# Kernel optimization log

Measured on AMD Instinct MI355X. Metric: run time of the kernel, lower is better.

## Reference

```python
import jax, jax.numpy as jnp
import numpy as np

B, N, T, E = 8, 10000, 12, 160000
C_IN, C_SP, C_OUT, K = 32, 64, 64, 3
EPS = 1e-5

def _conv1xk(x, w, b, pad):
    # x: (B, Cin, N, T), w: (Cout, Cin, 1, k) -- conv only along time axis
    y = jax.lax.conv_general_dilated(x, w, (1, 1), [(0, 0), (pad, pad)],
                                     dimension_numbers=('NCHW', 'OIHW', 'NCHW'))
    return y + b[None, :, None, None]

def _temporal_block(x, w, b, gamma, beta, mean, var):
    out = _conv1xk(x, w, b, pad=1)
    p, q = jnp.split(out, 2, axis=1)
    out = p * jax.nn.sigmoid(q)  # GLU gate
    scale = gamma * jax.lax.rsqrt(var + EPS)  # eval-mode BatchNorm2d
    return (out - mean[None, :, None, None]) * scale[None, :, None, None] + beta[None, :, None, None]

def _cheb_conv(x, edge_index, edge_weight, W, b):
    # x: (BT, N, C). PyG ChebConv, sym normalization, lambda_max=2 =>
    # Lhat = -D^{-1/2} A D^{-1/2} (zero diagonal). Recursion T0=x, T1=Lhat x,
    # Tk = 2 Lhat T_{k-1} - T_{k-2}; out = sum_k Tk @ W_k + b.
    row, col = edge_index[0], edge_index[1]
    n = x.shape[1]
    deg = jnp.zeros((n,), x.dtype).at[row].add(edge_weight)
    deg_safe = jnp.where(deg > 0, deg, 1.0)
    dinv = jnp.where(deg > 0, jax.lax.rsqrt(deg_safe), 0.0)
    norm = -edge_weight * dinv[row] * dinv[col]  # (E,)

    def lhat(z):
        msg = z[:, row, :] * norm[None, :, None]          # gather + scale
        return jnp.zeros_like(z).at[:, col, :].add(msg)   # scatter-add

    Tx0 = x
    out = jnp.einsum('bnc,cd->bnd', Tx0, W[0])
    Tx1 = lhat(x)
    out = out + jnp.einsum('bnc,cd->bnd', Tx1, W[1])
    for k in range(2, W.shape[0]):
        Tx2 = 2.0 * lhat(Tx1) - Tx0
        out = out + jnp.einsum('bnc,cd->bnd', Tx2, W[k])
        Tx0, Tx1 = Tx1, Tx2
    return out + b

def setup_inputs():
    key = jax.random.key(0)
    ks = jax.random.split(key, 16)
    s = 0.05
    return {
        'x': jax.random.normal(ks[0], (B, C_IN, N, T), jnp.float32),
        'edge_index': jax.random.randint(ks[1], (2, E), 0, N),
        'edge_weight': jax.random.uniform(ks[2], (E,), jnp.float32),
        'w_gate1': jax.random.normal(ks[3], (2 * C_SP, C_IN, 1, 3), jnp.float32) * s,
        'b_gate1': jnp.zeros((2 * C_SP,), jnp.float32),
        'bn1_gamma': 1.0 + 0.1 * jax.random.normal(ks[4], (C_SP,), jnp.float32),
        'bn1_beta': 0.1 * jax.random.normal(ks[5], (C_SP,), jnp.float32),
        'bn1_mean': 0.1 * jax.random.normal(ks[6], (C_SP,), jnp.float32),
        'bn1_var': jax.random.uniform(ks[7], (C_SP,), jnp.float32, 0.5, 1.5),
        'cheb_w': jax.random.normal(ks[8], (K, C_SP, C_SP), jnp.float32) * s,
        'cheb_b': jnp.zeros((C_SP,), jnp.float32),
        'ln_gamma': jnp.ones((C_SP,), jnp.float32),
        'ln_beta': jnp.zeros((C_SP,), jnp.float32),
        'w_gate2': jax.random.normal(ks[9], (2 * C_OUT, C_SP, 1, 3), jnp.float32) * s,
        'b_gate2': jnp.zeros((2 * C_OUT,), jnp.float32),
        'bn2_gamma': 1.0 + 0.1 * jax.random.normal(ks[10], (C_OUT,), jnp.float32),
        'bn2_beta': 0.1 * jax.random.normal(ks[11], (C_OUT,), jnp.float32),
        'bn2_mean': 0.1 * jax.random.normal(ks[12], (C_OUT,), jnp.float32),
        'bn2_var': jax.random.uniform(ks[13], (C_OUT,), jnp.float32, 0.5, 1.5),
        'w_res': jax.random.normal(ks[14], (C_OUT, C_IN, 1, 1), jnp.float32) * s,
        'b_res': jnp.zeros((C_OUT,), jnp.float32),
    }

def reference(x, edge_index, edge_weight, w_gate1, b_gate1, bn1_gamma, bn1_beta, bn1_mean, bn1_var,
              cheb_w, cheb_b, ln_gamma, ln_beta, w_gate2, b_gate2, bn2_gamma, bn2_beta, bn2_mean,
              bn2_var, w_res, b_res):
    b_, _, n_, t_ = x.shape
    res = _conv1xk(x, w_res, b_res, pad=0)  # 1x1 residual projection
    out = _temporal_block(x, w_gate1, b_gate1, bn1_gamma, bn1_beta, bn1_mean, bn1_var)
    c_s = out.shape[1]
    # (B, C_s, N, T) -> (B*T, N, C_s): spatial graph conv per time snapshot
    h = out.transpose(0, 3, 2, 1).reshape(b_ * t_, n_, c_s)
    h = _cheb_conv(h, edge_index, edge_weight, cheb_w, cheb_b)
    mu = h.mean(-1, keepdims=True)
    var = ((h - mu) ** 2).mean(-1, keepdims=True)
    h = (h - mu) * jax.lax.rsqrt(var + EPS) * ln_gamma + ln_beta  # LayerNorm
    h = jax.nn.relu(h)
    h = h.reshape(b_, t_, n_, c_s).transpose(0, 3, 2, 1)
    out = _temporal_block(h, w_gate2, b_gate2, bn2_gamma, bn2_beta, bn2_mean, bn2_var)
    return out + res
```

## Files before the change

kernel.cpp:

```cpp
#include <hip/hip_runtime.h>
#include <math.h>

#define BB 8
#define CIN 32
#define NN 10000
#define TTT 12
#define EE 160000
#define CSP 64
#define BT (BB*TTT)
#define NPAIR 48
#define EPSV 1e-5f

typedef __attribute__((ext_vector_type(8))) short bf16x8;
typedef __attribute__((ext_vector_type(4))) float f32x4;

static __device__ __forceinline__ float sigmoidf_(float v) {
    return __builtin_amdgcn_rcpf(1.f + __expf(-v));
}

static __device__ __forceinline__ short f2bf(float v) {
    unsigned u = __float_as_uint(v);
    u = (u + 0x7fffu + ((u >> 16) & 1u)) >> 16;
    return (short)u;
}
static __device__ __forceinline__ float lo16f(unsigned u) {
    return __uint_as_float(u << 16);
}
static __device__ __forceinline__ float hi16f(unsigned u) {
    return __uint_as_float(u & 0xffff0000u);
}
static __device__ __forceinline__ unsigned packbf(float a, float b) {
    return ((unsigned)(ushort)f2bf(a)) | (((unsigned)(ushort)f2bf(b)) << 16);
}

__global__ void k_deg(const int* __restrict__ ei, const float* __restrict__ ew,
                      float* __restrict__ deg) {
    int e = blockIdx.x * 256 + threadIdx.x;
    if (e < EE) atomicAdd(&deg[ei[e]], ew[e]);
}

__global__ void k_dinv(float* __restrict__ deg) {
    int n = blockIdx.x * 256 + threadIdx.x;
    if (n < NN) { float d = deg[n]; deg[n] = d > 0.f ? rsqrtf(d) : 0.f; }
}

__global__ void k_norm_cnt(const int* __restrict__ ei, const float* __restrict__ ew,
                           const float* __restrict__ dinv, float* __restrict__ nrm,
                           int* __restrict__ cnt) {
    int e = blockIdx.x * 256 + threadIdx.x;
    if (e < EE) {
        int r = ei[e], c = ei[EE + e];
        nrm[e] = -ew[e] * dinv[r] * dinv[c];
        atomicAdd(&cnt[c], 1);
    }
}

__global__ void k_scan(const int* __restrict__ cnt, int* __restrict__ offs,
                       int* __restrict__ cursor) {
    __shared__ int sh[1024];
    int tid = threadIdx.x;
    int running = 0;
    for (int base = 0; base < NN; base += 1024) {
        int i = base + tid;
        int v = (i < NN) ? cnt[i] : 0;
        sh[tid] = v;
        __syncthreads();
        for (int off = 1; off < 1024; off <<= 1) {
            int t = (tid >= off) ? sh[tid - off] : 0;
            __syncthreads();
            sh[tid] += t;
            __syncthreads();
        }
        int incl = sh[tid];
        if (i < NN) { offs[i] = running + incl - v; cursor[i] = running + incl - v; }
        int ct = sh[1023];
        __syncthreads();
        running += ct;
    }
    if (tid == 0) offs[NN] = running;
}

__global__ void k_fill(const int* __restrict__ ei, const float* __restrict__ nrm,
                       int* __restrict__ cursor, unsigned* __restrict__ csrp) {
    int e = blockIdx.x * 256 + threadIdx.x;
    if (e < EE) {
        int cdst = ei[EE + e];
        int p = atomicAdd(&cursor[cdst], 1);
        csrp[p] = (((unsigned)(ushort)f2bf(nrm[e])) << 16) | (unsigned)ei[e];
    }
}

__global__ void k_cvt_w(const float* __restrict__ wg1, const float* __restrict__ wg2,
                        const float* __restrict__ wr, const float* __restrict__ cwf,
                        short* __restrict__ wtap1, short* __restrict__ wtap2,
                        short* __restrict__ o3, short* __restrict__ wt02,
                        short* __restrict__ wt1, short* __restrict__ wt2) {
    int i = blockIdx.x * 256 + threadIdx.x;
    if (i < 12288) {
        int kk = i / 4096, r = i % 4096, cc = r >> 5, ci = r & 31;
        wtap1[i] = f2bf(wg1[cc * 96 + ci * 3 + kk]);
    }
    if (i < 24576) {
        int kk = i / 8192, r = i % 8192, cc = r >> 6, c = r & 63;
        wtap2[i] = f2bf(wg2[cc * 192 + c * 3 + kk]);
    }
    if (i < 2048)  o3[i] = f2bf(wr[i]);
    if (i < 4096) {
        int cout = i >> 6, cin = i & 63;
        float w0 = cwf[cin * 64 + cout];
        float w1 = cwf[4096 + cin * 64 + cout];
        float w2 = cwf[8192 + cin * 64 + cout];
        wt02[i] = f2bf(w0 - w2);
        wt1[i]  = f2bf(w1);
        wt2[i]  = f2bf(w2);
    }
}

__global__ __launch_bounds__(256, 6) void k_tconv1_mfma(
    const float* __restrict__ x, const short* __restrict__ wtap,
    const float* __restrict__ bg, const float* __restrict__ gam,
    const float* __restrict__ bet, const float* __restrict__ mean,
    const float* __restrict__ var, ushort* __restrict__ h1)
{
    __shared__ short Hs[4][14][40];
    int bi = blockIdx.x;
    int b = bi / 2500;
    int n0 = (bi % 2500) * 4;
    int tid = threadIdx.x;

    if (tid < 128) {
        int n = tid >> 5, ci = tid & 31;
        const float* xp = x + ((size_t)(b * CIN + ci) * NN + n0 + n) * 12;
        float4 a0 = *(const float4*)(xp);
        float4 a1 = *(const float4*)(xp + 4);
        float4 a2 = *(const float4*)(xp + 8);
        short* d = &Hs[n][0][ci];
        d[0] = 0; d[13 * 40] = 0;
        d[1 * 40] = f2bf(a0.x); d[2 * 40] = f2bf(a0.y); d[3 * 40] = f2bf(a0.z);
        d[4 * 40] = f2bf(a0.w); d[5 * 40] = f2bf(a1.x); d[6 * 40] = f2bf(a1.y);
        d[7 * 40] = f2bf(a1.z); d[8 * 40] = f2bf(a1.w); d[9 * 40] = f2bf(a2.x);
        d[10 * 40] = f2bf(a2.y); d[11 * 40] = f2bf(a2.z); d[12 * 40] = f2bf(a2.w);
    }
    __syncthreads();

    int w = tid >> 6, l = tid & 63, lr = l & 15, lq = l >> 4;
    int nct[3], tct[3];
#pragma unroll
    for (int ct = 0; ct < 3; ++ct) {
        int col = ct * 16 + lr;
        nct[ct] = col / 12; tct[ct] = col % 12;
    }
    f32x4 aP[3], aQ[3];
#pragma unroll
    for (int m = 0; m < 3; ++m) { aP[m] = (f32x4){0,0,0,0}; aQ[m] = (f32x4){0,0,0,0}; }

#pragma unroll
    for (int kk = 0; kk < 3; ++kk) {
        bf16x8 wp = *(const bf16x8*)(wtap + ((kk * 128 + w * 16 + lr) * 32 + lq * 8));
        bf16x8 wq = *(const bf16x8*)(wtap + ((kk * 128 + 64 + w * 16 + lr) * 32 + lq * 8));
#pragma unroll
        for (int ct = 0; ct < 3; ++ct) {
            bf16x8 im = *(const bf16x8*)&Hs[nct[ct]][tct[ct] + kk][lq * 8];
            aP[ct] = __builtin_amdgcn_mfma_f32_16x16x32_bf16(im, wp, aP[ct], 0, 0, 0);
            aQ[ct] = __builtin_amdgcn_mfma_f32_16x16x32_bf16(im, wq, aQ[ct], 0, 0, 0);
        }
    }

    int c = w * 16 + lr;
    float bp = bg[c], bq = bg[64 + c];
    float sc = gam[c] * rsqrtf(var[c] + EPSV);
    float mn = mean[c], be = bet[c];
#pragma unroll
    for (int mt = 0; mt < 3; ++mt) {
#pragma unroll
        for (int j = 0; j < 4; ++j) {
            int row = mt * 16 + lq * 4 + j;
            int n = n0 + row / 12, t = row % 12;
            float h = (aP[mt][j] + bp) * sigmoidf_(aQ[mt][j] + bq);
            h1[((size_t)(b * 6 + (t >> 1)) * NN + n) * 128 + (t & 1) * 64 + c] =
                (ushort)f2bf((h - mn) * sc + be);
        }
    }
}

__global__ __launch_bounds__(256, 8) void k_spatial(
    const ushort* __restrict__ h1, const int* __restrict__ offs,
    const unsigned* __restrict__ csr,
    const short* __restrict__ wt02, const short* __restrict__ wt1,
    const short* __restrict__ wt2, const float* __restrict__ cb,
    ushort* __restrict__ O, ushort* __restrict__ U)
{
    __shared__ short Al[64][72];
    __shared__ short Gl[64][72];
    int tid = threadIdx.x;
    int bi = blockIdx.x;
    int xcd = bi & 7, r = bi >> 3;
    int jp = r / 313, ck = r - jp * 313;
    int pair = xcd * 6 + jp;
    int n0 = ck * 32;

    const char* hp = (const char*)h1 + (size_t)pair * NN * 256;
    int w = tid >> 6, l = tid & 63;
    int snap = l >> 5, cp = l & 31;
    unsigned loff = (unsigned)(snap * 128 + cp * 4);

#pragma unroll
    for (int p = 0; p < 8; ++p) {
        int nl = p * 4 + w;
        int n = n0 + nl;
        float a0 = 0.f, a1 = 0.f, b0 = 0.f, b1 = 0.f;
        unsigned sv = 0;
        if (n < NN) {
            sv = *(const unsigned*)(hp + (((unsigned)n) << 8) + loff);
            int o0 = __builtin_amdgcn_readfirstlane(offs[n]);
            int o1 = __builtin_amdgcn_readfirstlane(offs[n + 1]);
            int i = o0;
            for (; i + 7 < o1; i += 8) {
                unsigned e0 = csr[i], e1 = csr[i+1], e2 = csr[i+2], e3 = csr[i+3];
                unsigned e4 = csr[i+4], e5 = csr[i+5], e6 = csr[i+6], e7 = csr[i+7];
                unsigned r0 = *(const unsigned*)(hp + ((e0 & 0xffffu) << 8) + loff);
                unsigned r1 = *(const unsigned*)(hp + ((e1 & 0xffffu) << 8) + loff);
                unsigned r2 = *(const unsigned*)(hp + ((e2 & 0xffffu) << 8) + loff);
                unsigned r3 = *(const unsigned*)(hp + ((e3 & 0xffffu) << 8) + loff);
                unsigned r4 = *(const unsigned*)(hp + ((e4 & 0xffffu) << 8) + loff);
                unsigned r5 = *(const unsigned*)(hp + ((e5 & 0xffffu) << 8) + loff);
                unsigned r6 = *(const unsigned*)(hp + ((e6 & 0xffffu) << 8) + loff);
                unsigned r7 = *(const unsigned*)(hp + ((e7 & 0xffffu) << 8) + loff);
                float w0 = hi16f(e0), w1 = hi16f(e1), w2 = hi16f(e2), w3 = hi16f(e3);
                float w4 = hi16f(e4), w5 = hi16f(e5), w6 = hi16f(e6), w7 = hi16f(e7);
                a0 = fmaf(w0, lo16f(r0), a0); a1 = fmaf(w0, hi16f(r0), a1);
                b0 = fmaf(w1, lo16f(r1), b0); b1 = fmaf(w1, hi16f(r1), b1);
                a0 = fmaf(w2, lo16f(r2), a0); a1 = fmaf(w2, hi16f(r2), a1);
                b0 = fmaf(w3, lo16f(r3), b0); b1 = fmaf(w3, hi16f(r3), b1);
                a0 = fmaf(w4, lo16f(r4), a0); a1 = fmaf(w4, hi16f(r4), a1);
                b0 = fmaf(w5, lo16f(r5), b0); b1 = fmaf(w5, hi16f(r5), b1);
                a0 = fmaf(w6, lo16f(r6), a0); a1 = fmaf(w6, hi16f(r6), a1);
                b0 = fmaf(w7, lo16f(r7), b0); b1 = fmaf(w7, hi16f(r7), b1);
            }
            for (; i + 3 < o1; i += 4) {
                unsigned e0 = csr[i], e1 = csr[i+1], e2 = csr[i+2], e3 = csr[i+3];
                unsigned r0 = *(const unsigned*)(hp + ((e0 & 0xffffu) << 8) + loff);
                unsigned r1 = *(const unsigned*)(hp + ((e1 & 0xffffu) << 8) + loff);
                unsigned r2 = *(const unsigned*)(hp + ((e2 & 0xffffu) << 8) + loff);
                unsigned r3 = *(const unsigned*)(hp + ((e3 & 0xffffu) << 8) + loff);
                float w0 = hi16f(e0), w1 = hi16f(e1), w2 = hi16f(e2), w3 = hi16f(e3);
                a0 = fmaf(w0, lo16f(r0), a0); a1 = fmaf(w0, hi16f(r0), a1);
                b0 = fmaf(w1, lo16f(r1), b0); b1 = fmaf(w1, hi16f(r1), b1);
                a0 = fmaf(w2, lo16f(r2), a0); a1 = fmaf(w2, hi16f(r2), a1);
                b0 = fmaf(w3, lo16f(r3), b0); b1 = fmaf(w3, hi16f(r3), b1);
            }
            for (; i < o1; ++i) {
                unsigned e = csr[i];
                unsigned rr = *(const unsigned*)(hp + ((e & 0xffffu) << 8) + loff);
                float ww = hi16f(e);
                a0 = fmaf(ww, lo16f(rr), a0); a1 = fmaf(ww, hi16f(rr), a1);
            }
        }
        int row = snap * 32 + nl;
        *(unsigned*)&Al[row][cp * 2] = sv;
        *(unsigned*)&Gl[row][cp * 2] = packbf(a0 + b0, a1 + b1);
    }
    __syncthreads();

    int lr = l & 15, lq = l >> 4;
    bf16x8 af[2], gf[2];
#pragma unroll
    for (int ks = 0; ks < 2; ++ks) {
        af[ks] = *(const bf16x8*)&Al[w * 16 + lr][ks * 32 + lq * 8];
        gf[ks] = *(const bf16x8*)&Gl[w * 16 + lr][ks * 32 + lq * 8];
    }
    f32x4 ao[4], au[4];
#pragma unroll
    for (int ct = 0; ct < 4; ++ct) { ao[ct] = (f32x4){0,0,0,0}; au[ct] = (f32x4){0,0,0,0}; }
#pragma unroll
    for (int ct = 0; ct < 4; ++ct) {
#pragma unroll
        for (int ks = 0; ks < 2; ++ks) {
            int woff = (ct * 16 + lr) * 64 + ks * 32 + lq * 8;
            bf16x8 b02 = *(const bf16x8*)(wt02 + woff);
            bf16x8 b1  = *(const bf16x8*)(wt1 + woff);
            bf16x8 b2  = *(const bf16x8*)(wt2 + woff);
            ao[ct] = __builtin_amdgcn_mfma_f32_16x16x32_bf16(af[ks], b02, ao[ct], 0, 0, 0);
            ao[ct] = __builtin_amdgcn_mfma_f32_16x16x32_bf16(gf[ks], b1,  ao[ct], 0, 0, 0);
            au[ct] = __builtin_amdgcn_mfma_f32_16x16x32_bf16(gf[ks], b2,  au[ct], 0, 0, 0);
        }
    }
    __syncthreads();

#pragma unroll
    for (int ct = 0; ct < 4; ++ct) {
        float bb = cb[ct * 16 + lr];
#pragma unroll
        for (int j2 = 0; j2 < 4; ++j2) {
            int rowo = w * 16 + lq * 4 + j2;
            Al[rowo][ct * 16 + lr] = f2bf(ao[ct][j2] + bb);
            Gl[rowo][ct * 16 + lr] = f2bf(au[ct][j2]);
        }
    }
    __syncthreads();

    size_t obase = (size_t)pair * NN * 128;
#pragma unroll
    for (int rr2 = 0; rr2 < 2; ++rr2) {
        int idx = tid + rr2 * 256;
        int node = idx >> 4, part = idx & 15;
        int sn = part >> 3, seg = part & 7;
        int n = n0 + node;
        if (n < NN) {
            size_t off = obase + (size_t)n * 128 + sn * 64 + seg * 8;
            __builtin_nontemporal_store(*(const bf16x8*)&Al[sn * 32 + node][seg * 8],
                                        (bf16x8*)(O + off));
            __builtin_nontemporal_store(*(const bf16x8*)&Gl[sn * 32 + node][seg * 8],
                                        (bf16x8*)(U + off));
        }
    }
}

__global__ __launch_bounds__(256, 8) void k_gather2_ln(
    const ushort* __restrict__ O, const ushort* __restrict__ U,
    const int* __restrict__ offs, const unsigned* __restrict__ csr,
    const float* __restrict__ lng, const float* __restrict__ lnb,
    ushort* __restrict__ hln)
{
    int bi = blockIdx.x;
    int xcd = bi & 7, r = bi >> 3;
    int jp = r / 625, ck = r - jp * 625;
    int pair = xcd * 6 + jp;
    int ng = ck * 16;
    int tid = threadIdx.x;
    int w = tid >> 6, l = tid & 63;
    int snap = l >> 5, cp = l & 31;
    unsigned loff = (unsigned)(snap * 128 + cp * 4);
    const char* up = (const char*)U + (size_t)pair * NN * 256;
    const char* op = (const char*)O + (size_t)pair * NN * 256;
    ushort* hlp = hln + (size_t)pair * NN * 128;

    float2 gv = ((const float2*)lng)[cp];
    float2 bv = ((const float2*)lnb)[cp];

#pragma unroll
    for (int p = 0; p < 4; ++p) {
        int n = ng + p * 4 + w;
        float a0 = 0.f, a1 = 0.f, b0 = 0.f, b1 = 0.f;
        int o0 = __builtin_amdgcn_readfirstlane(offs[n]);
        int o1 = __builtin_amdgcn_readfirstlane(offs[n + 1]);
        int i = o0;
        for (; i + 7 < o1; i += 8) {
            unsigned e0 = csr[i], e1 = csr[i+1], e2 = csr[i+2], e3 = csr[i+3];
            unsigned e4 = csr[i+4], e5 = csr[i+5], e6 = csr[i+6], e7 = csr[i+7];
            unsigned r0 = *(const unsigned*)(up + ((e0 & 0xffffu) << 8) + loff);
            unsigned r1 = *(const unsigned*)(up + ((e1 & 0xffffu) << 8) + loff);
            unsigned r2 = *(const unsigned*)(up + ((e2 & 0xffffu) << 8) + loff);
            unsigned r3 = *(const unsigned*)(up + ((e3 & 0xffffu) << 8) + loff);
            unsigned r4 = *(const unsigned*)(up + ((e4 & 0xffffu) << 8) + loff);
            unsigned r5 = *(const unsigned*)(up + ((e5 & 0xffffu) << 8) + loff);
            unsigned r6 = *(const unsigned*)(up + ((e6 & 0xffffu) << 8) + loff);
            unsigned r7 = *(const unsigned*)(up + ((e7 & 0xffffu) << 8) + loff);
            float w0 = hi16f(e0), w1 = hi16f(e1), w2 = hi16f(e2), w3 = hi16f(e3);
            float w4 = hi16f(e4), w5 = hi16f(e5), w6 = hi16f(e6), w7 = hi16f(e7);
            a0 = fmaf(w0, lo16f(r0), a0); a1 = fmaf(w0, hi16f(r0), a1);
            b0 = fmaf(w1, lo16f(r1), b0); b1 = fmaf(w1, hi16f(r1), b1);
            a0 = fmaf(w2, lo16f(r2), a0); a1 = fmaf(w2, hi16f(r2), a1);
            b0 = fmaf(w3, lo16f(r3), b0); b1 = fmaf(w3, hi16f(r3), b1);
            a0 = fmaf(w4, lo16f(r4), a0); a1 = fmaf(w4, hi16f(r4), a1);
            b0 = fmaf(w5, lo16f(r5), b0); b1 = fmaf(w5, hi16f(r5), b1);
            a0 = fmaf(w6, lo16f(r6), a0); a1 = fmaf(w6, hi16f(r6), a1);
            b0 = fmaf(w7, lo16f(r7), b0); b1 = fmaf(w7, hi16f(r7), b1);
        }
        for (; i + 3 < o1; i += 4) {
            unsigned e0 = csr[i], e1 = csr[i+1], e2 = csr[i+2], e3 = csr[i+3];
            unsigned r0 = *(const unsigned*)(up + ((e0 & 0xffffu) << 8) + loff);
            unsigned r1 = *(const unsigned*)(up + ((e1 & 0xffffu) << 8) + loff);
            unsigned r2 = *(const unsigned*)(up + ((e2 & 0xffffu) << 8) + loff);
            unsigned r3 = *(const unsigned*)(up + ((e3 & 0xffffu) << 8) + loff);
            float w0 = hi16f(e0), w1 = hi16f(e1), w2 = hi16f(e2), w3 = hi16f(e3);
            a0 = fmaf(w0, lo16f(r0), a0); a1 = fmaf(w0, hi16f(r0), a1);
            b0 = fmaf(w1, lo16f(r1), b0); b1 = fmaf(w1, hi16f(r1), b1);
            a0 = fmaf(w2, lo16f(r2), a0); a1 = fmaf(w2, hi16f(r2), a1);
            b0 = fmaf(w3, lo16f(r3), b0); b1 = fmaf(w3, hi16f(r3), b1);
        }
        for (; i < o1; ++i) {
            unsigned e = csr[i];
            unsigned rr = *(const unsigned*)(up + ((e & 0xffffu) << 8) + loff);
            float ww = hi16f(e);
            a0 = fmaf(ww, lo16f(rr), a0); a1 = fmaf(ww, hi16f(rr), a1);
        }
        unsigned ov = *(const unsigned*)(op + (((unsigned)n) << 8) + loff);
        float acc0 = lo16f(ov) + 2.f * (a0 + b0);
        float acc1 = hi16f(ov) + 2.f * (a1 + b1);
        float s1 = acc0 + acc1;
        float s2 = acc0 * acc0 + acc1 * acc1;
#pragma unroll
        for (int m = 16; m >= 1; m >>= 1) {
            s1 += __shfl_xor(s1, m);
            s2 += __shfl_xor(s2, m);
        }
        float mu = s1 * (1.f / 64.f);
        float vr = s2 * (1.f / 64.f) - mu * mu;
        float rstd = rsqrtf(vr + EPSV);
        float y0 = fmaxf((acc0 - mu) * rstd * gv.x + bv.x, 0.f);
        float y1 = fmaxf((acc1 - mu) * rstd * gv.y + bv.y, 0.f);
        __builtin_nontemporal_store(packbf(y0, y1),
            (unsigned*)(hlp + (size_t)n * 128 + snap * 64 + cp * 2));
    }
}

__global__ __launch_bounds__(256, 4) void k_tconv2_mfma(
    const ushort* __restrict__ hln, const float* __restrict__ x,
    const short* __restrict__ wtap, const short* __restrict__ wrbf,
    const float* __restrict__ bg, const float* __restrict__ gam,
    const float* __restrict__ bet, const float* __restrict__ mean,
    const float* __restrict__ var, const float* __restrict__ bres,
    float* __restrict__ out)
{
    __shared__ short Hs[4][14][72];
    __shared__ short Bx[48 * 40];
    int bi = blockIdx.x;
    int b = bi / 2500;
    int n0 = (bi % 2500) * 4;
    int tid = threadIdx.x;

    for (int j = tid; j < 384; j += 256) {
        int n = j / 96, rem = j % 96;
        int p = rem >> 4, seg = rem & 15;
        bf16x8 v = *(const bf16x8*)(hln + ((size_t)(b * 6 + p) * NN + n0 + n) * 128 + seg * 8);
        *(bf16x8*)&Hs[n][1 + 2 * p + (seg >> 3)][(seg & 7) * 8] = v;
    }
    if (tid < 64) {
        int n = tid >> 4, pt = tid & 15;
        bf16x8 z = (bf16x8){0,0,0,0,0,0,0,0};
        *(bf16x8*)&Hs[n][(pt >> 3) * 13][(pt & 7) * 8] = z;
    }
    for (int j = tid; j < 384; j += 256) {
        int ci = j / 12, r = j - ci * 12;
        const float* xp = x + ((size_t)(b * CIN + ci) * NN + n0) * 12 + r * 4;
        float4 v = *(const float4*)xp;
        float vv[4] = {v.x, v.y, v.z, v.w};
#pragma unroll
        for (int e = 0; e < 4; ++e) {
            int col = r * 4 + e;
            Bx[col * 40 + ci] = f2bf(vv[e]);
        }
    }
    __syncthreads();

    int w = tid >> 6, l = tid & 63, lr = l & 15, lq = l >> 4;
    int nct[3], tct[3];
#pragma unroll
    for (int ct = 0; ct < 3; ++ct) {
        int col = ct * 16 + lr;
        nct[ct] = col / 12; tct[ct] = col % 12;
    }
    f32x4 accP[3], accQ[3], accR[3];
#pragma unroll
    for (int m = 0; m < 3; ++m) {
        accP[m] = (f32x4){0,0,0,0}; accQ[m] = (f32x4){0,0,0,0}; accR[m] = (f32x4){0,0,0,0};
    }

#pragma unroll
    for (int kk = 0; kk < 3; ++kk) {
#pragma unroll
        for (int ks = 0; ks < 2; ++ks) {
            bf16x8 aP = *(const bf16x8*)(wtap + ((kk * 128 + w * 16 + lr) * 64 + ks * 32 + lq * 8));
            bf16x8 aQ = *(const bf16x8*)(wtap + ((kk * 128 + 64 + w * 16 + lr) * 64 + ks * 32 + lq * 8));
#pragma unroll
            for (int ct = 0; ct < 3; ++ct) {
                bf16x8 bfr = *(const bf16x8*)&Hs[nct[ct]][tct[ct] + kk][ks * 32 + lq * 8];
                accP[ct] = __builtin_amdgcn_mfma_f32_16x16x32_bf16(aP, bfr, accP[ct], 0, 0, 0);
                accQ[ct] = __builtin_amdgcn_mfma_f32_16x16x32_bf16(aQ, bfr, accQ[ct], 0, 0, 0);
            }
        }
    }
    {
        bf16x8 aR = *(const bf16x8*)(wrbf + ((w * 16 + lr) * 32 + lq * 8));
#pragma unroll
        for (int ct = 0; ct < 3; ++ct) {
            bf16x8 bx = *(const bf16x8*)(&Bx[(ct * 16 + lr) * 40 + lq * 8]);
            accR[ct] = __builtin_amdgcn_mfma_f32_16x16x32_bf16(aR, bx, accR[ct], 0, 0, 0);
        }
    }

    float bpv[4], bqv[4], scv[4], mnv[4], bev[4], brv[4];
#pragma unroll
    for (int j = 0; j < 4; ++j) {
        int cj = w * 16 + lq * 4 + j;
        bpv[j] = bg[cj]; bqv[j] = bg[64 + cj];
        scv[j] = gam[cj] * rsqrtf(var[cj] + EPSV);
        mnv[j] = mean[cj]; bev[j] = bet[cj]; brv[j] = bres[cj];
    }
#pragma unroll
    for (int ct = 0; ct < 3; ++ct) {
        int col = ct * 16 + lr;
        int n = n0 + col / 12, t = col % 12;
#pragma unroll
        for (int j = 0; j < 4; ++j) {
            int cj = w * 16 + lq * 4 + j;
            float h = (accP[ct][j] + bpv[j]) * sigmoidf_(accQ[ct][j] + bqv[j]);
            float o = (h - mnv[j]) * scv[j] + bev[j] + accR[ct][j] + brv[j];
            __builtin_nontemporal_store(o, &out[((size_t)(b * 64 + cj) * NN + n) * 12 + t]);
        }
    }
}

extern "C" void kernel_launch(void* const* d_in, const int* in_sizes, int n_in,
                              void* d_out, int out_size, void* d_ws, size_t ws_size,
                              hipStream_t stream)
{
    const float* x   = (const float*)d_in[0];
    const int*   ei  = (const int*)d_in[1];
    const float* ew  = (const float*)d_in[2];
    const float* wg1 = (const float*)d_in[3];
    const float* bg1 = (const float*)d_in[4];
    const float* g1  = (const float*)d_in[5];
    const float* be1 = (const float*)d_in[6];
    const float* m1  = (const float*)d_in[7];
    const float* v1  = (const float*)d_in[8];
    const float* cw  = (const float*)d_in[9];
    const float* cb  = (const float*)d_in[10];
    const float* lng = (const float*)d_in[11];
    const float* lnb = (const float*)d_in[12];
    const float* wg2 = (const float*)d_in[13];
    const float* bg2 = (const float*)d_in[14];
    const float* g2  = (const float*)d_in[15];
    const float* be2 = (const float*)d_in[16];
    const float* m2  = (const float*)d_in[17];
    const float* v2  = (const float*)d_in[18];
    const float* wr  = (const float*)d_in[19];
    const float* br  = (const float*)d_in[20];

    char* w = (char*)d_ws;
    short* wtap1 = (short*)w;  w += 12288 * 2;
    short* wtap2 = (short*)w;  w += 24576 * 2;
    short* wrbf  = (short*)w;  w += 2048 * 2;
    short* wt02  = (short*)w;  w += 4096 * 2;
    short* wt1   = (short*)w;  w += 4096 * 2;
    short* wt2   = (short*)w;  w += 4096 * 2;
    ushort* h1   = (ushort*)w; w += (size_t)NPAIR * NN * 128 * 2;
    ushort* O    = (ushort*)w; w += (size_t)NPAIR * NN * 128 * 2;
    float* deg   = (float*)w;  w += NN * 4;
    int*   cnt   = (int*)w;    w += NN * 4;
    int*   offs  = (int*)w;    w += (NN + 1) * 4;
    int*   cursor= (int*)w;    w += NN * 4;
    float* nrm   = (float*)w;  w += EE * 4;
    unsigned* csr = (unsigned*)w; w += EE * 4;
    ushort* U = (ushort*)d_out;

    hipMemsetAsync(deg, 0, NN * 4 * 2, stream);

    k_deg<<<625, 256, 0, stream>>>(ei, ew, deg);
    k_dinv<<<40, 256, 0, stream>>>(deg);
    k_norm_cnt<<<625, 256, 0, stream>>>(ei, ew, deg, nrm, cnt);
    k_scan<<<1, 1024, 0, stream>>>(cnt, offs, cursor);
    k_fill<<<625, 256, 0, stream>>>(ei, nrm, cursor, csr);
    k_cvt_w<<<96, 256, 0, stream>>>(wg1, wg2, wr, cw, wtap1, wtap2, wrbf, wt02, wt1, wt2);

    k_tconv1_mfma<<<BB * 2500, 256, 0, stream>>>(x, wtap1, bg1, g1, be1, m1, v1, h1);
    k_spatial<<<8 * 6 * 313, 256, 0, stream>>>(h1, offs, csr, wt02, wt1, wt2, cb, O, U);
    k_gather2_ln<<<8 * 6 * 625, 256, 0, stream>>>(O, U, offs, csr, lng, lnb, h1);
    k_tconv2_mfma<<<BB * 2500, 256, 0, stream>>>(h1, x, wtap2, wrbf, bg2, g2, be2, m2, v2, br,
                                                 (float*)d_out);
}
```

Measured before the change: 818.5 us.

## Split edge neighbors across wave halves with 8-byte row gathers

Result: slower. 906.7 us (+10.8%).

```diff
diff --git a/kernel.cpp b/kernel.cpp
--- a/kernel.cpp
+++ b/kernel.cpp
@@ -183,6 +183,24 @@
     }
 }
 
+#define PAIR2(PTR, PV, A0, A1, A2, A3)                                        \
+    {                                                                          \
+        unsigned e = half ? (PV).y : (PV).x;                                   \
+        uint2 rv = *(const uint2*)((PTR) + ((e & 0xffffu) << 8) + loff2);      \
+        float ww = hi16f(e);                                                   \
+        A0 = fmaf(ww, lo16f(rv.x), A0); A1 = fmaf(ww, hi16f(rv.x), A1);        \
+        A2 = fmaf(ww, lo16f(rv.y), A2); A3 = fmaf(ww, hi16f(rv.y), A3);        \
+    }
+
+#define SINGLE1(PTR, I, A0, A1, A2, A3)                                       \
+    {                                                                          \
+        unsigned e = csr[I];                                                   \
+        uint2 rv = *(const uint2*)((PTR) + ((e & 0xffffu) << 8) + loff2);      \
+        float ww = half ? 0.f : hi16f(e);                                      \
+        A0 = fmaf(ww, lo16f(rv.x), A0); A1 = fmaf(ww, hi16f(rv.x), A1);        \
+        A2 = fmaf(ww, lo16f(rv.y), A2); A3 = fmaf(ww, hi16f(rv.y), A3);        \
+    }
+
 __global__ __launch_bounds__(256, 8) void k_spatial(
     const ushort* __restrict__ h1, const int* __restrict__ offs,
     const unsigned* __restrict__ csr,
@@ -201,64 +219,49 @@
 
     const char* hp = (const char*)h1 + (size_t)pair * NN * 256;
     int w = tid >> 6, l = tid & 63;
-    int snap = l >> 5, cp = l & 31;
-    unsigned loff = (unsigned)(snap * 128 + cp * 4);
+    int half = l >> 5, sub = l & 31;
+    unsigned loff2 = (unsigned)(sub * 8);
 
 #pragma unroll
     for (int p = 0; p < 8; ++p) {
         int nl = p * 4 + w;
         int n = n0 + nl;
-        float a0 = 0.f, a1 = 0.f, b0 = 0.f, b1 = 0.f;
-        unsigned sv = 0;
+        float a0 = 0.f, a1 = 0.f, a2 = 0.f, a3 = 0.f;
+        float b0 = 0.f, b1 = 0.f, b2 = 0.f, b3 = 0.f;
+        uint2 sv = {0u, 0u};
         if (n < NN) {
-            sv = *(const unsigned*)(hp + (((unsigned)n) << 8) + loff);
-            int o0 = __builtin_amdgcn_readfirstlane(offs[n]);
+            sv = *(const uint2*)(hp + (((unsigned)n) << 8) + loff2);
+            int i  = __builtin_amdgcn_readfirstlane(offs[n]);
             int o1 = __builtin_amdgcn_readfirstlane(offs[n + 1]);
-            int i = o0;
+            if ((i & 1) && i < o1) { SINGLE1(hp, i, a0, a1, a2, a3); ++i; }
             for (; i + 7 < o1; i += 8) {
-                unsigned e0 = csr[i], e1 = csr[i+1], e2 = csr[i+2], e3 = csr[i+3];
-                unsigned e4 = csr[i+4], e5 = csr[i+5], e6 = csr[i+6], e7 = csr[i+7];
-                unsigned r0 = *(const unsigned*)(hp + ((e0 & 0xffffu) << 8) + loff);
-                unsigned r1 = *(const unsigned*)(hp + ((e1 & 0xffffu) << 8) + loff);
-                unsigned r2 = *(const unsigned*)(hp + ((e2 & 0xffffu) << 8) + loff);
-                unsigned r3 = *(const unsigned*)(hp + ((e3 & 0xffffu) << 8) + loff);
-                unsigned r4 = *(const unsigned*)(hp + ((e4 & 0xffffu) << 8) + loff);
-                unsigned r5 = *(const unsigned*)(hp + ((e5 & 0xffffu) << 8) + loff);
-                unsigned r6 = *(const unsigned*)(hp + ((e6 & 0xffffu) << 8) + loff);
-                unsigned r7 = *(const unsigned*)(hp + ((e7 & 0xffffu) << 8) + loff);
-                float w0 = hi16f(e0), w1 = hi16f(e1), w2 = hi16f(e2), w3 = hi16f(e3);
-                float w4 = hi16f(e4), w5 = hi16f(e5), w6 = hi16f(e6), w7 = hi16f(e7);
-                a0 = fmaf(w0, lo16f(r0), a0); a1 = fmaf(w0, hi16f(r0), a1);
-                b0 = fmaf(w1, lo16f(r1), b0); b1 = fmaf(w1, hi16f(r1), b1);
-                a0 = fmaf(w2, lo16f(r2), a0); a1 = fmaf(w2, hi16f(r2), a1);
-                b0 = fmaf(w3, lo16f(r3), b0); b1 = fmaf(w3, hi16f(r3), b1);
-                a0 = fmaf(w4, lo16f(r4), a0); a1 = fmaf(w4, hi16f(r4), a1);
-                b0 = fmaf(w5, lo16f(r5), b0); b1 = fmaf(w5, hi16f(r5), b1);
-                a0 = fmaf(w6, lo16f(r6), a0); a1 = fmaf(w6, hi16f(r6), a1);
-                b0 = fmaf(w7, lo16f(r7), b0); b1 = fmaf(w7, hi16f(r7), b1);
+                uint2 p0 = *(const uint2*)(csr + i);
+                uint2 p1 = *(const uint2*)(csr + i + 2);
+                uint2 p2 = *(const uint2*)(csr + i + 4);
+                uint2 p3 = *(const uint2*)(csr + i + 6);
+                PAIR2(hp, p0, a0, a1, a2, a3);
+                PAIR2(hp, p1, b0, b1, b2, b3);
+                PAIR2(hp, p2, a0, a1, a2, a3);
+                PAIR2(hp, p3, b0, b1, b2, b3);
             }
-            for (; i + 3 < o1; i += 4) {
-                unsigned e0 = csr[i], e1 = csr[i+1], e2 = csr[i+2], e3 = csr[i+3];
-                unsigned r0 = *(const unsigned*)(hp + ((e0 & 0xffffu) << 8) + loff);
-                unsigned r1 = *(const unsigned*)(hp + ((e1 & 0xffffu) << 8) + loff);
-                unsigned r2 = *(const unsigned*)(hp + ((e2 & 0xffffu) << 8) + loff);
-                unsigned r3 = *(const unsigned*)(hp + ((e3 & 0xffffu) << 8) + loff);
-                float w0 = hi16f(e0), w1 = hi16f(e1), w2 = hi16f(e2), w3 = hi16f(e3);
-                a0 = fmaf(w0, lo16f(r0), a0); a1 = fmaf(w0, hi16f(r0), a1);
-                b0 = fmaf(w1, lo16f(r1), b0); b1 = fmaf(w1, hi16f(r1), b1);
-                a0 = fmaf(w2, lo16f(r2), a0); a1 = fmaf(w2, hi16f(r2), a1);
-                b0 = fmaf(w3, lo16f(r3), b0); b1 = fmaf(w3, hi16f(r3), b1);
+            for (; i + 1 < o1; i += 2) {
+                uint2 p0 = *(const uint2*)(csr + i);
+                PAIR2(hp, p0, a0, a1, a2, a3);
             }
-            for (; i < o1; ++i) {
-                unsigned e = csr[i];
-                unsigned rr = *(const unsigned*)(hp + ((e & 0xffffu) << 8) + loff);
-                float ww = hi16f(e);
-                a0 = fmaf(ww, lo16f(rr), a0); a1 = fmaf(ww, hi16f(rr), a1);
-            }
-        }
-        int row = snap * 32 + nl;
-        *(unsigned*)&Al[row][cp * 2] = sv;
-        *(unsigned*)&Gl[row][cp * 2] = packbf(a0 + b0, a1 + b1);
+            if (i < o1) SINGLE1(hp, i, a0, a1, a2, a3);
+        }
+        float t0 = a0 + b0, t1 = a1 + b1, t2 = a2 + b2, t3 = a3 + b3;
+        t0 += __shfl_xor(t0, 32);
+        t1 += __shfl_xor(t1, 32);
+        t2 += __shfl_xor(t2, 32);
+        t3 += __shfl_xor(t3, 32);
+        if (half == 0) {
+            int rowo = (sub >> 4) * 32 + nl;
+            int chg = sub & 15;
+            *(uint2*)&Al[rowo][chg * 4] = sv;
+            uint2 gp = { packbf(t0, t1), packbf(t2, t3) };
+            *(uint2*)&Gl[rowo][chg * 4] = gp;
+        }
     }
     __syncthreads();
 
@@ -329,79 +332,72 @@
     int ng = ck * 16;
     int tid = threadIdx.x;
     int w = tid >> 6, l = tid & 63;
-    int snap = l >> 5, cp = l & 31;
-    unsigned loff = (unsigned)(snap * 128 + cp * 4);
+    int half = l >> 5, sub = l & 31;
+    unsigned loff2 = (unsigned)(sub * 8);
     const char* up = (const char*)U + (size_t)pair * NN * 256;
     const char* op = (const char*)O + (size_t)pair * NN * 256;
     ushort* hlp = hln + (size_t)pair * NN * 128;
 
-    float2 gv = ((const float2*)lng)[cp];
-    float2 bv = ((const float2*)lnb)[cp];
+    int c0i = sub * 2;
+    float2 gva = ((const float2*)lng)[c0i & 31];
+    float2 gvb = ((const float2*)lng)[(c0i + 1) & 31];
+    float2 bva = ((const float2*)lnb)[c0i & 31];
+    float2 bvb = ((const float2*)lnb)[(c0i + 1) & 31];
 
 #pragma unroll
     for (int p = 0; p < 4; ++p) {
         int n = ng + p * 4 + w;
-        float a0 = 0.f, a1 = 0.f, b0 = 0.f, b1 = 0.f;
-        int o0 = __builtin_amdgcn_readfirstlane(offs[n]);
+        float a0 = 0.f, a1 = 0.f, a2 = 0.f, a3 = 0.f;
+        float b0 = 0.f, b1 = 0.f, b2 = 0.f, b3 = 0.f;
+        int i  = __builtin_amdgcn_readfirstlane(offs[n]);
         int o1 = __builtin_amdgcn_readfirstlane(offs[n + 1]);
-        int i = o0;
+        if ((i & 1) && i < o1) { SINGLE1(up, i, a0, a1, a2, a3); ++i; }
         for (; i + 7 < o1; i += 8) {
-            unsigned e0 = csr[i], e1 = csr[i+1], e2 = csr[i+2], e3 = csr[i+3];
-            unsigned e4 = csr[i+4], e5 = csr[i+5], e6 = csr[i+6], e7 = csr[i+7];
-            unsigned r0 = *(const unsigned*)(up + ((e0 & 0xffffu) << 8) + loff);
-            unsigned r1 = *(const unsigned*)(up + ((e1 & 0xffffu) << 8) + loff);
-            unsigned r2 = *(const unsigned*)(up + ((e2 & 0xffffu) << 8) + loff);
-            unsigned r3 = *(const unsigned*)(up + ((e3 & 0xffffu) << 8) + loff);
-            unsigned r4 = *(const unsigned*)(up + ((e4 & 0xffffu) << 8) + loff);
-            unsigned r5 = *(const unsigned*)(up + ((e5 & 0xffffu) << 8) + loff);
-            unsigned r6 = *(const unsigned*)(up + ((e6 & 0xffffu) << 8) + loff);
-            unsigned r7 = *(const unsigned*)(up + ((e7 & 0xffffu) << 8) + loff);
-            float w0 = hi16f(e0), w1 = hi16f(e1), w2 = hi16f(e2), w3 = hi16f(e3);
-            float w4 = hi16f(e4), w5 = hi16f(e5), w6 = hi16f(e6), w7 = hi16f(e7);
-            a0 = fmaf(w0, lo16f(r0), a0); a1 = fmaf(w0, hi16f(r0), a1);
-            b0 = fmaf(w1, lo16f(r1), b0); b1 = fmaf(w1, hi16f(r1), b1);
-            a0 = fmaf(w2, lo16f(r2), a0); a1 = fmaf(w2, hi16f(r2), a1);
-            b0 = fmaf(w3, lo16f(r3), b0); b1 = fmaf(w3, hi16f(r3), b1);
-            a0 = fmaf(w4, lo16f(r4), a0); a1 = fmaf(w4, hi16f(r4), a1);
-            b0 = fmaf(w5, lo16f(r5), b0); b1 = fmaf(w5, hi16f(r5), b1);
-            a0 = fmaf(w6, lo16f(r6), a0); a1 = fmaf(w6, hi16f(r6), a1);
-            b0 = fmaf(w7, lo16f(r7), b0); b1 = fmaf(w7, hi16f(r7), b1);
-        }
-        for (; i + 3 < o1; i += 4) {
-            unsigned e0 = csr[i], e1 = csr[i+1], e2 = csr[i+2], e3 = csr[i+3];
-            unsigned r0 = *(const unsigned*)(up + ((e0 & 0xffffu) << 8) + loff);
-            unsigned r1 = *(const unsigned*)(up + ((e1 & 0xffffu) << 8) + loff);
-            unsigned r2 = *(const unsigned*)(up + ((e2 & 0xffffu) << 8) + loff);
-            unsigned r3 = *(const unsigned*)(up + ((e3 & 0xffffu) << 8) + loff);
-            float w0 = hi16f(e0), w1 = hi16f(e1), w2 = hi16f(e2), w3 = hi16f(e3);
-            a0 = fmaf(w0, lo16f(r0), a0); a1 = fmaf(w0, hi16f(r0), a1);
-            b0 = fmaf(w1, lo16f(r1), b0); b1 = fmaf(w1, hi16f(r1), b1);
-            a0 = fmaf(w2, lo16f(r2), a0); a1 = fmaf(w2, hi16f(r2), a1);
-            b0 = fmaf(w3, lo16f(r3), b0); b1 = fmaf(w3, hi16f(r3), b1);
-        }
-        for (; i < o1; ++i) {
-            unsigned e = csr[i];
-            unsigned rr = *(const unsigned*)(up + ((e & 0xffffu) << 8) + loff);
-            float ww = hi16f(e);
-            a0 = fmaf(ww, lo16f(rr), a0); a1 = fmaf(ww, hi16f(rr), a1);
-        }
-        unsigned ov = *(const unsigned*)(op + (((unsigned)n) << 8) + loff);
-        float acc0 = lo16f(ov) + 2.f * (a0 + b0);
-        float acc1 = hi16f(ov) + 2.f * (a1 + b1);
-        float s1 = acc0 + acc1;
-        float s2 = acc0 * acc0 + acc1 * acc1;
-#pragma unroll
-        for (int m = 16; m >= 1; m >>= 1) {
+            uint2 p0 = *(const uint2*)(csr + i);
+            uint2 p1 = *(const uint2*)(csr + i + 2);
+            uint2 p2 = *(const uint2*)(csr + i + 4);
+            uint2 p3 = *(const uint2*)(csr + i + 6);
+            PAIR2(up, p0, a0, a1, a2, a3);
+            PAIR2(up, p1, b0, b1, b2, b3);
+            PAIR2(up, p2, a0, a1, a2, a3);
+            PAIR2(up, p3, b0, b1, b2, b3);
+        }
+        for (; i + 1 < o1; i += 2) {
+            uint2 p0 = *(const uint2*)(csr + i);
+            PAIR2(up, p0, a0, a1, a2, a3);
+        }
+        if (i < o1) SINGLE1(up, i, a0, a1, a2, a3);
+
+        float g0 = a0 + b0, g1 = a1 + b1, g2 = a2 + b2, g3 = a3 + b3;
+        g0 += __shfl_xor(g0, 32);
+        g1 += __shfl_xor(g1, 32);
+        g2 += __shfl_xor(g2, 32);
+        g3 += __shfl_xor(g3, 32);
+
+        uint2 ov = *(const uint2*)(op + (((unsigned)n) << 8) + loff2);
+        float acc0 = lo16f(ov.x) + 2.f * g0;
+        float acc1 = hi16f(ov.x) + 2.f * g1;
+        float acc2 = lo16f(ov.y) + 2.f * g2;
+        float acc3 = hi16f(ov.y) + 2.f * g3;
+        float s1 = (acc0 + acc1) + (acc2 + acc3);
+        float s2 = (acc0 * acc0 + acc1 * acc1) + (acc2 * acc2 + acc3 * acc3);
+#pragma unroll
+        for (int m = 8; m >= 1; m >>= 1) {
             s1 += __shfl_xor(s1, m);
             s2 += __shfl_xor(s2, m);
         }
         float mu = s1 * (1.f / 64.f);
         float vr = s2 * (1.f / 64.f) - mu * mu;
         float rstd = rsqrtf(vr + EPSV);
-        float y0 = fmaxf((acc0 - mu) * rstd * gv.x + bv.x, 0.f);
-        float y1 = fmaxf((acc1 - mu) * rstd * gv.y + bv.y, 0.f);
-        __builtin_nontemporal_store(packbf(y0, y1),
-            (unsigned*)(hlp + (size_t)n * 128 + snap * 64 + cp * 2));
+        float y0 = fmaxf((acc0 - mu) * rstd * gva.x + bva.x, 0.f);
+        float y1 = fmaxf((acc1 - mu) * rstd * gva.y + bva.y, 0.f);
+        float y2 = fmaxf((acc2 - mu) * rstd * gvb.x + bvb.x, 0.f);
+        float y3 = fmaxf((acc3 - mu) * rstd * gvb.y + bvb.y, 0.f);
+        if (half == 0) {
+            uint2 pk = { packbf(y0, y1), packbf(y2, y3) };
+            __builtin_nontemporal_store(*(unsigned long long*)&pk,
+                (unsigned long long*)(hlp + (size_t)n * 128 + sub * 4));
+        }
     }
 }
 
@@ -542,6 +538,7 @@
     int*   offs  = (int*)w;    w += (NN + 1) * 4;
     int*   cursor= (int*)w;    w += NN * 4;
     float* nrm   = (float*)w;  w += EE * 4;
+    w = (char*)(((size_t)w + 15) & ~(size_t)15);
     unsigned* csr = (unsigned*)w; w += EE * 4;
     ushort* U = (ushort*)d_out;
 
```
